# Kernel tuning notes

Measured on AMD Instinct MI355X. Metric: run time of the kernel, lower is better.

## Reference

```python
import jax, jax.numpy as jnp
import numpy as np

T_TYPES, N_ARGS, N_MAPS = 15, 73, 3
D, H, FF = 512, 8, 512
N_TOK = 3071
LN_EPS = 1e-5


def setup_inputs() -> dict:
    key = jax.random.key(0)
    ks = jax.random.split(key, 32)
    s = 0.02
    p = lambda i, shape: (jax.random.normal(ks[i], shape, dtype=jnp.float32) * s)
    inp = {
        'subtask_index_history': jax.random.randint(ks[0], (N_TOK,), 0, T_TYPES * N_ARGS * N_MAPS, dtype=jnp.int32),
        'seq_masks': jax.random.randint(ks[1], (N_TOK,), 0, 64, dtype=jnp.int32),
        'Wt': p(2, (D, T_TYPES)), 'bt': p(3, (D,)),
        'Wa': p(4, (D, N_ARGS)), 'ba': p(5, (D,)),
        'Wm': p(6, (D, N_MAPS)), 'bm': p(7, (D,)),
        'sos': jnp.zeros((D,), dtype=jnp.float32),
        'Wq': p(8, (D, D)), 'bq': p(9, (D,)),
        'Wk': p(10, (D, D)), 'bk': p(11, (D,)),
        'Wv': p(12, (D, D)), 'bv': p(13, (D,)),
        'Wo': p(14, (D, D)), 'bo': p(15, (D,)),
        'W1': p(16, (FF, D)), 'b1': p(17, (FF,)),
        'W2': p(18, (D, FF)), 'b2': p(19, (D,)),
        'g1': jnp.ones((D,), jnp.float32), 'be1': jnp.zeros((D,), jnp.float32),
        'g2': jnp.ones((D,), jnp.float32), 'be2': jnp.zeros((D,), jnp.float32),
    }
    return inp


def _layer_norm(x, g, b):
    mu = jnp.mean(x, axis=-1, keepdims=True)
    var = jnp.mean((x - mu) ** 2, axis=-1, keepdims=True)
    return (x - mu) * jax.lax.rsqrt(var + LN_EPS) * g + b


def _enc_layer(x, mask, Wq, bq, Wk, bk, Wv, bv, Wo, bo, W1, b1, W2, b2, g1, be1, g2, be2):
    # x: [L, D]; mask: [L, L] additive (0 / -inf). inputs_are_labels=True -> no attn residual.
    L = x.shape[0]
    dh = D // H
    q = (x @ Wq.T + bq).reshape(L, H, dh)
    k = (x @ Wk.T + bk).reshape(L, H, dh)
    v = (x @ Wv.T + bv).reshape(L, H, dh)
    scores = jnp.einsum('ihd,jhd->hij', q, k) / np.sqrt(dh) + mask[None]  # [H, L, L]
    pr = jax.nn.softmax(scores, axis=-1)
    o = jnp.einsum('hij,jhd->ihd', pr, v).reshape(L, D)
    a = o @ Wo.T + bo
    xa = _layer_norm(a, g1, be1)
    y = jax.nn.leaky_relu(xa @ W1.T + b1) @ W2.T + b2
    return _layer_norm(xa + y, g2, be2)


def reference(subtask_index_history, seq_masks, Wt, bt, Wa, ba, Wm, bm, sos,
              Wq, bq, Wk, bk, Wv, bv, Wo, bo, W1, b1, W2, b2, g1, be1, g2, be2):
    idx = subtask_index_history
    t = idx // (N_ARGS * N_MAPS)
    a = (idx // N_MAPS) % N_ARGS
    m = idx % N_MAPS
    # one-hot @ Linear == embedding gather + bias
    emb = (Wt.T[t] + bt) + (Wa.T[a] + ba) + (Wm.T[m] + bm)  # [N, D]
    x = jnp.concatenate([sos[None, :], emb], axis=0)  # [L, D]
    L = x.shape[0]
    batch_ids = jnp.cumsum((seq_masks == 0).astype(jnp.int32))
    bid = jnp.concatenate([jnp.array([-1], jnp.int32), batch_ids])  # SOS gets unique id
    ar = jnp.arange(L)
    allowed = (ar[None, :] == 0) | ((bid[:, None] == bid[None, :]) & (ar[None, :] < ar[:, None]))
    mask = jnp.where(allowed, 0.0, -jnp.inf).astype(jnp.float32)
    lp = (Wq, bq, Wk, bk, Wv, bv, Wo, bo, W1, b1, W2, b2, g1, be1, g2, be2)
    # original reuses transformer_layer_a for both calls
    x = _enc_layer(x, mask, *lp)
    x = _enc_layer(x, mask, *lp)
    return x
```

## Files before the change

kernel.cpp:

```cpp
#include <hip/hip_runtime.h>

typedef unsigned short ushort_t;
typedef unsigned int uint_t;

#define L_TOK 3072
#define DMODEL 512
#define WELEM 262144

using bf16x8 = __attribute__((ext_vector_type(8))) short;
using f32x4  = __attribute__((ext_vector_type(4))) float;

__device__ __forceinline__ float b2f(ushort_t u) {
    union { uint_t i; float f; } c; c.i = ((uint_t)u) << 16; return c.f;
}
__device__ __forceinline__ ushort_t f2b(float f) {
    union { float f; uint_t i; } c; c.f = f;
    uint_t x = c.i;
    return (ushort_t)((x + 0x7fffu + ((x >> 16) & 1u)) >> 16);
}

__global__ __launch_bounds__(256) void prologue_kernel(
    const float* __restrict__ Wq, const float* __restrict__ Wk, const float* __restrict__ Wv,
    const float* __restrict__ Wo, const float* __restrict__ W1, const float* __restrict__ W2,
    ushort_t* __restrict__ WB,
    const int* __restrict__ idx,
    const float* __restrict__ Wt, const float* __restrict__ bt,
    const float* __restrict__ Wa, const float* __restrict__ ba,
    const float* __restrict__ Wm, const float* __restrict__ bm,
    const float* __restrict__ sos, ushort_t* __restrict__ X,
    const int* __restrict__ seq, int* __restrict__ start)
{
    __shared__ int sbuf0[256];
    __shared__ int sbuf1[256];
    int bid = blockIdx.x;
    int tid = threadIdx.x;

    if (bid < 1536) {
        int gid = bid * 256 + tid;
        int mat = gid >> 16;
        int off = (gid & 65535) * 4;
        const float* src;
        switch (mat) {
            case 0: src = Wq; break;
            case 1: src = Wk; break;
            case 2: src = Wv; break;
            case 3: src = Wo; break;
            case 4: src = W1; break;
            default: src = W2; break;
        }
        float4 v = *reinterpret_cast<const float4*>(src + off);
        uint2 o;
        o.x = (uint_t)f2b(v.x) | ((uint_t)f2b(v.y) << 16);
        o.y = (uint_t)f2b(v.z) | ((uint_t)f2b(v.w) << 16);
        *reinterpret_cast<uint2*>(&WB[mat * WELEM + off]) = o;
    } else if (bid < 7680) {
        int gid = (bid - 1536) * 256 + tid;
        int tok = gid >> 9;
        int d = gid & 511;
        float val;
        if (tok == 0) {
            val = sos[d];
        } else {
            int id = idx[tok - 1];
            int t = id / 219;
            int a = (id / 3) % 73;
            int m = id % 3;
            val = Wt[d * 15 + t] + bt[d]
                + Wa[d * 73 + a] + ba[d]
                + Wm[d * 3 + m] + bm[d];
        }
        X[gid] = f2b(val);
    } else {
        int carry = 0;
        for (int c = 0; c < 12; c++) {
            int i = c * 256 + tid;
            int b;
            if (i <= 1) b = i;
            else b = (seq[i - 1] == 0) ? i : 0;
            sbuf0[tid] = b;
            __syncthreads();
            int* src = sbuf0;
            int* dst = sbuf1;
            for (int off = 1; off < 256; off <<= 1) {
                int v = src[tid];
                if (tid >= off) { int u = src[tid - off]; if (u > v) v = u; }
                dst[tid] = v;
                __syncthreads();
                int* t = src; src = dst; dst = t;
            }
            int val = src[tid] > carry ? src[tid] : carry;
            start[i] = val;
            int tot = src[255] > carry ? src[255] : carry;
            __syncthreads();
            carry = tot;
        }
    }
}

template<int RELU>
__global__ __launch_bounds__(256) void gemm512(
    const ushort_t* __restrict__ A,
    const ushort_t* __restrict__ Wp0, const ushort_t* __restrict__ Wp1, const ushort_t* __restrict__ Wp2,
    const float* __restrict__ bp0, const float* __restrict__ bp1, const float* __restrict__ bp2,
    ushort_t* __restrict__ Cp0, ushort_t* __restrict__ Cp1, ushort_t* __restrict__ Cp2)
{
    const ushort_t* W = Wp0; const float* bias = bp0; ushort_t* C = Cp0;
    if (blockIdx.z == 1) { W = Wp1; bias = bp1; C = Cp1; }
    else if (blockIdx.z == 2) { W = Wp2; bias = bp2; C = Cp2; }

    __shared__ ushort_t As[64 * 72];
    __shared__ ushort_t Bs[64 * 72];

    const int tid = threadIdx.x;
    const int lane = tid & 63;
    const int w = tid >> 6;
    const int lm = lane & 15;
    const int q4 = lane >> 4;

    const int m0 = blockIdx.x * 64;
    const int n0 = blockIdx.y * 64;

    f32x4 acc[4];
#pragma unroll
    for (int i = 0; i < 4; i++) acc[i] = (f32x4){0.f, 0.f, 0.f, 0.f};

    for (int k0 = 0; k0 < 512; k0 += 64) {
        for (int c = tid; c < 512; c += 256) {
            int row = c >> 3, col = (c & 7) << 3;
            uint4 va = *reinterpret_cast<const uint4*>(&A[(size_t)(m0 + row) * 512 + k0 + col]);
            *reinterpret_cast<uint4*>(&As[row * 72 + col]) = va;
            uint4 vb = *reinterpret_cast<const uint4*>(&W[(size_t)(n0 + row) * 512 + k0 + col]);
            *reinterpret_cast<uint4*>(&Bs[row * 72 + col]) = vb;
        }
        __syncthreads();
#pragma unroll
        for (int kk = 0; kk < 64; kk += 32) {
            bf16x8 af = *reinterpret_cast<const bf16x8*>(&As[(w * 16 + lm) * 72 + kk + q4 * 8]);
#pragma unroll
            for (int nt = 0; nt < 4; nt++) {
                bf16x8 bf = *reinterpret_cast<const bf16x8*>(&Bs[(nt * 16 + lm) * 72 + kk + q4 * 8]);
                acc[nt] = __builtin_amdgcn_mfma_f32_16x16x32_bf16(af, bf, acc[nt], 0, 0, 0);
            }
        }
        __syncthreads();
    }

#pragma unroll
    for (int nt = 0; nt < 4; nt++) {
        int col = n0 + nt * 16 + lm;
        float bv = bias[col];
#pragma unroll
        for (int r = 0; r < 4; r++) {
            int row = m0 + w * 16 + q4 * 4 + r;
            float v = acc[nt][r] + bv;
            if (RELU) v = (v > 0.f) ? v : 0.01f * v;
            C[(size_t)row * 512 + col] = f2b(v);
        }
    }
}

__global__ __launch_bounds__(256) void attn_mfma(
    const ushort_t* __restrict__ Q, const ushort_t* __restrict__ K,
    const ushort_t* __restrict__ V, const int* __restrict__ START,
    ushort_t* __restrict__ O)
{
    __shared__ ushort_t VtS[4][64 * 72];
    __shared__ ushort_t PsS[4][16 * 72];

    int w = threadIdx.x >> 6;
    int lane = threadIdx.x & 63;
    ushort_t* Vt = VtS[w];
    ushort_t* Ps = PsS[w];

    int gw = blockIdx.x * 4 + w;
    int tile = 191 - (gw >> 3);
    int h = gw & 7;
    int i0 = tile * 16;
    int lm = lane & 15;
    int q4 = lane >> 4;

    int iq0 = i0 + q4 * 4;
    int sq[4];
#pragma unroll
    for (int r = 0; r < 4; r++) sq[r] = START[iq0 + r];

    int lo = START[i0]; if (lo < 1) lo = 1;
    int nk = i0 + 16 - lo;

    const ushort_t* Qp = Q + (size_t)(i0 + lm) * 512 + h * 64 + q4 * 8;
    bf16x8 aQ0 = *reinterpret_cast<const bf16x8*>(Qp);
    bf16x8 aQ1 = *reinterpret_cast<const bf16x8*>(Qp + 32);

    float m_run[4], l_run[4];
    f32x4 oacc[4];
#pragma unroll
    for (int r = 0; r < 4; r++) { m_run[r] = -INFINITY; l_run[r] = 0.f; }
#pragma unroll
    for (int nt = 0; nt < 4; nt++) oacc[nt] = (f32x4){0.f, 0.f, 0.f, 0.f};

    for (int t0 = 0; t0 < nk; t0 += 64) {
        int tv = t0 + lane;
        int jv = (tv == 0) ? 0 : (lo + tv - 1);
        if (jv > L_TOK - 1) jv = L_TOK - 1;
        const uint4* vp = reinterpret_cast<const uint4*>(&V[(size_t)jv * 512 + h * 64]);
        uint4 vr[8];
#pragma unroll
        for (int c = 0; c < 8; c++) vr[c] = vp[c];

        int jn[4];
#pragma unroll
        for (int nt = 0; nt < 4; nt++) {
            int t = t0 + nt * 16 + lm;
            jn[nt] = (t == 0) ? 0 : (lo + t - 1);
        }
        f32x4 sacc[4];
#pragma unroll
        for (int nt = 0; nt < 4; nt++) sacc[nt] = (f32x4){0.f, 0.f, 0.f, 0.f};
#pragma unroll
        for (int nt = 0; nt < 4; nt++) {
            int jc = jn[nt] > L_TOK - 1 ? L_TOK - 1 : jn[nt];
            const ushort_t* Kp = K + (size_t)jc * 512 + h * 64 + q4 * 8;
            bf16x8 bK0 = *reinterpret_cast<const bf16x8*>(Kp);
            bf16x8 bK1 = *reinterpret_cast<const bf16x8*>(Kp + 32);
            sacc[nt] = __builtin_amdgcn_mfma_f32_16x16x32_bf16(aQ0, bK0, sacc[nt], 0, 0, 0);
            sacc[nt] = __builtin_amdgcn_mfma_f32_16x16x32_bf16(aQ1, bK1, sacc[nt], 0, 0, 0);
        }

#pragma unroll
        for (int c = 0; c < 8; c++) {
            uint_t ww[4] = {vr[c].x, vr[c].y, vr[c].z, vr[c].w};
#pragma unroll
            for (int e = 0; e < 4; e++) {
                int d0 = c * 8 + e * 2;
                Vt[d0 * 72 + lane] = (ushort_t)(ww[e] & 0xffffu);
                Vt[(d0 + 1) * 72 + lane] = (ushort_t)(ww[e] >> 16);
            }
        }

#pragma unroll
        for (int nt = 0; nt < 4; nt++) {
            int jju = jn[nt];
#pragma unroll
            for (int r = 0; r < 4; r++) {
                float s = sacc[nt][r] * 0.125f;
                bool val = (jju == 0) || (sq[r] <= jju && jju < iq0 + r);
                sacc[nt][r] = val ? s : -INFINITY;
            }
        }

        float mnew[4], alpha[4];
#pragma unroll
        for (int r = 0; r < 4; r++) {
            float mx = fmaxf(fmaxf(sacc[0][r], sacc[1][r]), fmaxf(sacc[2][r], sacc[3][r]));
            mx = fmaxf(mx, __shfl_xor(mx, 1));
            mx = fmaxf(mx, __shfl_xor(mx, 2));
            mx = fmaxf(mx, __shfl_xor(mx, 4));
            mx = fmaxf(mx, __shfl_xor(mx, 8));
            float mn = fmaxf(m_run[r], mx);
            mnew[r] = mn;
            alpha[r] = __expf(m_run[r] - mn);
        }

#pragma unroll
        for (int r = 0; r < 4; r++) {
            float rs = 0.f;
#pragma unroll
            for (int nt = 0; nt < 4; nt++) {
                float p = __expf(sacc[nt][r] - mnew[r]);
                rs += p;
                Ps[(q4 * 4 + r) * 72 + nt * 16 + lm] = f2b(p);
            }
            rs += __shfl_xor(rs, 1);
            rs += __shfl_xor(rs, 2);
            rs += __shfl_xor(rs, 4);
            rs += __shfl_xor(rs, 8);
            l_run[r] = l_run[r] * alpha[r] + rs;
            m_run[r] = mnew[r];
        }
#pragma unroll
        for (int nt = 0; nt < 4; nt++)
#pragma unroll
            for (int r = 0; r < 4; r++) oacc[nt][r] *= alpha[r];

        bf16x8 aP0 = *reinterpret_cast<const bf16x8*>(&Ps[lm * 72 + q4 * 8]);
        bf16x8 aP1 = *reinterpret_cast<const bf16x8*>(&Ps[lm * 72 + 32 + q4 * 8]);
#pragma unroll
        for (int nt = 0; nt < 4; nt++) {
            bf16x8 bV0 = *reinterpret_cast<const bf16x8*>(&Vt[(nt * 16 + lm) * 72 + q4 * 8]);
            bf16x8 bV1 = *reinterpret_cast<const bf16x8*>(&Vt[(nt * 16 + lm) * 72 + 32 + q4 * 8]);
            oacc[nt] = __builtin_amdgcn_mfma_f32_16x16x32_bf16(aP0, bV0, oacc[nt], 0, 0, 0);
            oacc[nt] = __builtin_amdgcn_mfma_f32_16x16x32_bf16(aP1, bV1, oacc[nt], 0, 0, 0);
        }
    }

#pragma unroll
    for (int r = 0; r < 4; r++) {
        float inv = (l_run[r] > 0.f) ? (1.f / l_run[r]) : 0.f;
#pragma unroll
        for (int nt = 0; nt < 4; nt++)
            O[(size_t)(iq0 + r) * 512 + h * 64 + nt * 16 + lm] = f2b(oacc[nt][r] * inv);
    }
}

template<int RESID, int F32OUT>
__global__ __launch_bounds__(256) void ln_kernel(
    const ushort_t* __restrict__ X, const ushort_t* __restrict__ R,
    const float* __restrict__ g, const float* __restrict__ be,
    void* __restrict__ outv)
{
    int tok = blockIdx.x * 4 + (threadIdx.x >> 6);
    int lane = threadIdx.x & 63;
    size_t base = (size_t)tok * 512 + lane * 8;

    float v[8];
    {
        uint4 ux = *reinterpret_cast<const uint4*>(&X[base]);
        uint_t ua[4] = {ux.x, ux.y, ux.z, ux.w};
#pragma unroll
        for (int p = 0; p < 4; p++) {
            v[2 * p] = b2f((ushort_t)(ua[p] & 0xffffu));
            v[2 * p + 1] = b2f((ushort_t)(ua[p] >> 16));
        }
        if (RESID) {
            uint4 ur = *reinterpret_cast<const uint4*>(&R[base]);
            uint_t ub[4] = {ur.x, ur.y, ur.z, ur.w};
#pragma unroll
            for (int p = 0; p < 4; p++) {
                v[2 * p] += b2f((ushort_t)(ub[p] & 0xffffu));
                v[2 * p + 1] += b2f((ushort_t)(ub[p] >> 16));
            }
        }
    }
    float sum = 0.f;
#pragma unroll
    for (int j = 0; j < 8; j++) sum += v[j];
#pragma unroll
    for (int off = 32; off > 0; off >>= 1) sum += __shfl_xor(sum, off);
    float mu = sum * (1.f / 512.f);
    float var = 0.f;
#pragma unroll
    for (int j = 0; j < 8; j++) { float d = v[j] - mu; var += d * d; }
#pragma unroll
    for (int off = 32; off > 0; off >>= 1) var += __shfl_xor(var, off);
    float rstd = rsqrtf(var * (1.f / 512.f) + 1e-5f);

    const float4* gp = reinterpret_cast<const float4*>(g);
    const float4* bp = reinterpret_cast<const float4*>(be);
    float4 g0 = gp[2 * lane], g1 = gp[2 * lane + 1];
    float4 b0 = bp[2 * lane], b1 = bp[2 * lane + 1];
    float gg[8] = {g0.x, g0.y, g0.z, g0.w, g1.x, g1.y, g1.z, g1.w};
    float bb[8] = {b0.x, b0.y, b0.z, b0.w, b1.x, b1.y, b1.z, b1.w};

    float o[8];
#pragma unroll
    for (int j = 0; j < 8; j++) o[j] = (v[j] - mu) * rstd * gg[j] + bb[j];

    if (F32OUT) {
        float* outf = (float*)outv;
        float4 o0 = {o[0], o[1], o[2], o[3]};
        float4 o1 = {o[4], o[5], o[6], o[7]};
        *reinterpret_cast<float4*>(&outf[base]) = o0;
        *reinterpret_cast<float4*>(&outf[base + 4]) = o1;
    } else {
        ushort_t* outb = (ushort_t*)outv;
        uint_t outp[4];
#pragma unroll
        for (int p = 0; p < 4; p++)
            outp[p] = (uint_t)f2b(o[2 * p]) | ((uint_t)f2b(o[2 * p + 1]) << 16);
        uint4 ov; ov.x = outp[0]; ov.y = outp[1]; ov.z = outp[2]; ov.w = outp[3];
        *reinterpret_cast<uint4*>(&outb[base]) = ov;
    }
}

extern "C" void kernel_launch(void* const* d_in, const int* in_sizes, int n_in,
                              void* d_out, int out_size, void* d_ws, size_t ws_size,
                              hipStream_t stream) {
    const int*   idx = (const int*)d_in[0];
    const int*   seq = (const int*)d_in[1];
    const float* Wt  = (const float*)d_in[2];
    const float* bt  = (const float*)d_in[3];
    const float* Wa  = (const float*)d_in[4];
    const float* ba  = (const float*)d_in[5];
    const float* Wm  = (const float*)d_in[6];
    const float* bm  = (const float*)d_in[7];
    const float* sos = (const float*)d_in[8];
    const float* Wq  = (const float*)d_in[9];
    const float* bq  = (const float*)d_in[10];
    const float* Wk  = (const float*)d_in[11];
    const float* bk  = (const float*)d_in[12];
    const float* Wv  = (const float*)d_in[13];
    const float* bv  = (const float*)d_in[14];
    const float* Wo  = (const float*)d_in[15];
    const float* bo  = (const float*)d_in[16];
    const float* W1  = (const float*)d_in[17];
    const float* b1  = (const float*)d_in[18];
    const float* W2  = (const float*)d_in[19];
    const float* b2  = (const float*)d_in[20];
    const float* g1  = (const float*)d_in[21];
    const float* be1 = (const float*)d_in[22];
    const float* g2  = (const float*)d_in[23];
    const float* be2 = (const float*)d_in[24];

    const size_t NB = (size_t)L_TOK * DMODEL;

    int* START = (int*)d_ws;
    ushort_t* WB = (ushort_t*)d_ws + 16384;
    ushort_t* WQc = WB + 0 * WELEM;
    ushort_t* WKc = WB + 1 * WELEM;
    ushort_t* WVc = WB + 2 * WELEM;
    ushort_t* WOc = WB + 3 * WELEM;
    ushort_t* W1c = WB + 4 * WELEM;
    ushort_t* W2c = WB + 5 * WELEM;
    ushort_t* bufs = WB + 6 * WELEM;
    ushort_t* B0 = bufs;
    ushort_t* B1 = bufs + 1 * NB;
    ushort_t* B2 = bufs + 2 * NB;
    ushort_t* B3 = bufs + 3 * NB;

    prologue_kernel<<<7681, 256, 0, stream>>>(
        Wq, Wk, Wv, Wo, W1, W2, WB,
        idx, Wt, bt, Wa, ba, Wm, bm, sos, B0,
        seq, START);

    for (int layer = 0; layer < 2; layer++) {
        gemm512<0><<<dim3(48, 8, 3), 256, 0, stream>>>(B0, WQc, WKc, WVc, bq, bk, bv, B1, B2, B3);
        attn_mfma<<<384, 256, 0, stream>>>(B1, B2, B3, START, B0);
        gemm512<0><<<dim3(48, 8, 1), 256, 0, stream>>>(B0, WOc, WOc, WOc, bo, bo, bo, B1, B1, B1);
        ln_kernel<0, 0><<<768, 256, 0, stream>>>(B1, B1, g1, be1, B2);
        gemm512<1><<<dim3(48, 8, 1), 256, 0, stream>>>(B2, W1c, W1c, W1c, b1, b1, b1, B1, B1, B1);
        gemm512<0><<<dim3(48, 8, 1), 256, 0, stream>>>(B1, W2c, W2c, W2c, b2, b2, b2, B3, B3, B3);
        if (layer == 0)
            ln_kernel<1, 0><<<768, 256, 0, stream>>>(B3, B2, g2, be2, B0);
        else
            ln_kernel<1, 1><<<768, 256, 0, stream>>>(B3, B2, g2, be2, d_out);
    }
}
```

Baseline: 275.5 us.

## Double-buffer LDS tiles in gemm512 with register prefetch of next K tile

The GEMM kernel now keeps two LDS buffers for A and W tiles. It prefetches the next K-slice from global memory into registers while MFMAs run on the current buffer, then writes it to the alternate buffer. This removes one barrier per K iteration and hides global load latency behind compute. In exchange it doubles shared memory per block and uses more registers, which may reduce occupancy.

```diff
diff --git a/kernel.cpp b/kernel.cpp
--- a/kernel.cpp
+++ b/kernel.cpp
@@ -108,8 +108,8 @@
     if (blockIdx.z == 1) { W = Wp1; bias = bp1; C = Cp1; }
     else if (blockIdx.z == 2) { W = Wp2; bias = bp2; C = Cp2; }
 
-    __shared__ ushort_t As[64 * 72];
-    __shared__ ushort_t Bs[64 * 72];
+    __shared__ ushort_t As[2 * 64 * 72];
+    __shared__ ushort_t Bs[2 * 64 * 72];
 
     const int tid = threadIdx.x;
     const int lane = tid & 63;
@@ -120,29 +120,60 @@
     const int m0 = blockIdx.x * 64;
     const int n0 = blockIdx.y * 64;
 
+    const int row0 = tid >> 3;
+    const int colc = (tid & 7) << 3;
+    const ushort_t* Arow0 = A + (size_t)(m0 + row0) * 512 + colc;
+    const ushort_t* Arow1 = Arow0 + (size_t)32 * 512;
+    const ushort_t* Brow0 = W + (size_t)(n0 + row0) * 512 + colc;
+    const ushort_t* Brow1 = Brow0 + (size_t)32 * 512;
+    const int lds0 = row0 * 72 + colc;
+    const int lds1 = (row0 + 32) * 72 + colc;
+
     f32x4 acc[4];
 #pragma unroll
     for (int i = 0; i < 4; i++) acc[i] = (f32x4){0.f, 0.f, 0.f, 0.f};
 
-    for (int k0 = 0; k0 < 512; k0 += 64) {
-        for (int c = tid; c < 512; c += 256) {
-            int row = c >> 3, col = (c & 7) << 3;
-            uint4 va = *reinterpret_cast<const uint4*>(&A[(size_t)(m0 + row) * 512 + k0 + col]);
-            *reinterpret_cast<uint4*>(&As[row * 72 + col]) = va;
-            uint4 vb = *reinterpret_cast<const uint4*>(&W[(size_t)(n0 + row) * 512 + k0 + col]);
-            *reinterpret_cast<uint4*>(&Bs[row * 72 + col]) = vb;
-        }
-        __syncthreads();
+    uint4 a0 = *reinterpret_cast<const uint4*>(Arow0);
+    uint4 a1 = *reinterpret_cast<const uint4*>(Arow1);
+    uint4 b0 = *reinterpret_cast<const uint4*>(Brow0);
+    uint4 b1 = *reinterpret_cast<const uint4*>(Brow1);
+    *reinterpret_cast<uint4*>(&As[lds0]) = a0;
+    *reinterpret_cast<uint4*>(&As[lds1]) = a1;
+    *reinterpret_cast<uint4*>(&Bs[lds0]) = b0;
+    *reinterpret_cast<uint4*>(&Bs[lds1]) = b1;
+    __syncthreads();
+
+#pragma unroll
+    for (int it = 0; it < 8; it++) {
+        const int cur = (it & 1) * 4608;
+        const int alt = ((it & 1) ^ 1) * 4608;
+        const int nxt = (it + 1) * 64;
+
+        uint4 na0, na1, nb0, nb1;
+        if (it < 7) {
+            na0 = *reinterpret_cast<const uint4*>(Arow0 + nxt);
+            na1 = *reinterpret_cast<const uint4*>(Arow1 + nxt);
+            nb0 = *reinterpret_cast<const uint4*>(Brow0 + nxt);
+            nb1 = *reinterpret_cast<const uint4*>(Brow1 + nxt);
+        }
+
 #pragma unroll
         for (int kk = 0; kk < 64; kk += 32) {
-            bf16x8 af = *reinterpret_cast<const bf16x8*>(&As[(w * 16 + lm) * 72 + kk + q4 * 8]);
+            bf16x8 af = *reinterpret_cast<const bf16x8*>(&As[cur + (w * 16 + lm) * 72 + kk + q4 * 8]);
 #pragma unroll
             for (int nt = 0; nt < 4; nt++) {
-                bf16x8 bf = *reinterpret_cast<const bf16x8*>(&Bs[(nt * 16 + lm) * 72 + kk + q4 * 8]);
+                bf16x8 bf = *reinterpret_cast<const bf16x8*>(&Bs[cur + (nt * 16 + lm) * 72 + kk + q4 * 8]);
                 acc[nt] = __builtin_amdgcn_mfma_f32_16x16x32_bf16(af, bf, acc[nt], 0, 0, 0);
             }
         }
-        __syncthreads();
+
+        if (it < 7) {
+            *reinterpret_cast<uint4*>(&As[alt + lds0]) = na0;
+            *reinterpret_cast<uint4*>(&As[alt + lds1]) = na1;
+            *reinterpret_cast<uint4*>(&Bs[alt + lds0]) = nb0;
+            *reinterpret_cast<uint4*>(&Bs[alt + lds1]) = nb1;
+            __syncthreads();
+        }
     }
 
 #pragma unroll
```

Result: faster. 253.9 us (-7.8%).

## Double-buffer GEMM LDS tiles with register prefetch and shrink M tile to 32

Applied to the files above, without the earlier changes.

The 512-K GEMM now prefetches the next K-slice from global memory into registers while MFMAs run on the current LDS buffer, then writes it into an alternate LDS buffer. This leaves one barrier per iteration instead of two. The block tile shrinks from 64x64 to 32x64, with each wave computing a 16x32 sub-tile, so twice as many blocks launch for better occupancy on the small 3072-row problem. In exchange, LDS use rises and each block does fewer MFMAs per B-tile load, which lowers reuse.

```diff
diff --git a/kernel.cpp b/kernel.cpp
--- a/kernel.cpp
+++ b/kernel.cpp
@@ -108,50 +108,81 @@
     if (blockIdx.z == 1) { W = Wp1; bias = bp1; C = Cp1; }
     else if (blockIdx.z == 2) { W = Wp2; bias = bp2; C = Cp2; }
 
-    __shared__ ushort_t As[64 * 72];
-    __shared__ ushort_t Bs[64 * 72];
+    __shared__ ushort_t As[2 * 32 * 72];
+    __shared__ ushort_t Bs[2 * 64 * 72];
 
     const int tid = threadIdx.x;
     const int lane = tid & 63;
     const int w = tid >> 6;
     const int lm = lane & 15;
     const int q4 = lane >> 4;
-
-    const int m0 = blockIdx.x * 64;
+    const int r0 = (w & 1) * 16;
+    const int c0 = (w >> 1) * 32;
+
+    const int m0 = blockIdx.x * 32;
     const int n0 = blockIdx.y * 64;
 
-    f32x4 acc[4];
-#pragma unroll
-    for (int i = 0; i < 4; i++) acc[i] = (f32x4){0.f, 0.f, 0.f, 0.f};
-
-    for (int k0 = 0; k0 < 512; k0 += 64) {
-        for (int c = tid; c < 512; c += 256) {
-            int row = c >> 3, col = (c & 7) << 3;
-            uint4 va = *reinterpret_cast<const uint4*>(&A[(size_t)(m0 + row) * 512 + k0 + col]);
-            *reinterpret_cast<uint4*>(&As[row * 72 + col]) = va;
-            uint4 vb = *reinterpret_cast<const uint4*>(&W[(size_t)(n0 + row) * 512 + k0 + col]);
-            *reinterpret_cast<uint4*>(&Bs[row * 72 + col]) = vb;
-        }
-        __syncthreads();
+    const int srow = tid >> 3;
+    const int scol = (tid & 7) << 3;
+    const ushort_t* Arow = A + (size_t)(m0 + srow) * 512 + scol;
+    const ushort_t* Brow0 = W + (size_t)(n0 + srow) * 512 + scol;
+    const ushort_t* Brow1 = Brow0 + (size_t)32 * 512;
+    const int ldsA = srow * 72 + scol;
+    const int ldsB0 = srow * 72 + scol;
+    const int ldsB1 = (srow + 32) * 72 + scol;
+
+    f32x4 acc[2];
+    acc[0] = (f32x4){0.f, 0.f, 0.f, 0.f};
+    acc[1] = (f32x4){0.f, 0.f, 0.f, 0.f};
+
+    uint4 a0 = *reinterpret_cast<const uint4*>(Arow);
+    uint4 b0 = *reinterpret_cast<const uint4*>(Brow0);
+    uint4 b1 = *reinterpret_cast<const uint4*>(Brow1);
+    *reinterpret_cast<uint4*>(&As[ldsA]) = a0;
+    *reinterpret_cast<uint4*>(&Bs[ldsB0]) = b0;
+    *reinterpret_cast<uint4*>(&Bs[ldsB1]) = b1;
+    __syncthreads();
+
+#pragma unroll
+    for (int it = 0; it < 8; it++) {
+        const int curA = (it & 1) * 2304;
+        const int altA = ((it & 1) ^ 1) * 2304;
+        const int curB = (it & 1) * 4608;
+        const int altB = ((it & 1) ^ 1) * 4608;
+        const int nxt = (it + 1) * 64;
+
+        uint4 na, nb0, nb1;
+        if (it < 7) {
+            na = *reinterpret_cast<const uint4*>(Arow + nxt);
+            nb0 = *reinterpret_cast<const uint4*>(Brow0 + nxt);
+            nb1 = *reinterpret_cast<const uint4*>(Brow1 + nxt);
+        }
+
 #pragma unroll
         for (int kk = 0; kk < 64; kk += 32) {
-            bf16x8 af = *reinterpret_cast<const bf16x8*>(&As[(w * 16 + lm) * 72 + kk + q4 * 8]);
-#pragma unroll
-            for (int nt = 0; nt < 4; nt++) {
-                bf16x8 bf = *reinterpret_cast<const bf16x8*>(&Bs[(nt * 16 + lm) * 72 + kk + q4 * 8]);
+            bf16x8 af = *reinterpret_cast<const bf16x8*>(&As[curA + (r0 + lm) * 72 + kk + q4 * 8]);
+#pragma unroll
+            for (int nt = 0; nt < 2; nt++) {
+                bf16x8 bf = *reinterpret_cast<const bf16x8*>(&Bs[curB + (c0 + nt * 16 + lm) * 72 + kk + q4 * 8]);
                 acc[nt] = __builtin_amdgcn_mfma_f32_16x16x32_bf16(af, bf, acc[nt], 0, 0, 0);
             }
         }
-        __syncthreads();
-    }
-
-#pragma unroll
-    for (int nt = 0; nt < 4; nt++) {
-        int col = n0 + nt * 16 + lm;
+
+        if (it < 7) {
+            *reinterpret_cast<uint4*>(&As[altA + ldsA]) = na;
+            *reinterpret_cast<uint4*>(&Bs[altB + ldsB0]) = nb0;
+            *reinterpret_cast<uint4*>(&Bs[altB + ldsB1]) = nb1;
+            __syncthreads();
+        }
+    }
+
+#pragma unroll
+    for (int nt = 0; nt < 2; nt++) {
+        int col = n0 + c0 + nt * 16 + lm;
         float bv = bias[col];
 #pragma unroll
         for (int r = 0; r < 4; r++) {
-            int row = m0 + w * 16 + q4 * 4 + r;
+            int row = m0 + r0 + q4 * 4 + r;
             float v = acc[nt][r] + bv;
             if (RELU) v = (v > 0.f) ? v : 0.01f * v;
             C[(size_t)row * 512 + col] = f2b(v);
@@ -423,12 +454,12 @@
         seq, START);
 
     for (int layer = 0; layer < 2; layer++) {
-        gemm512<0><<<dim3(48, 8, 3), 256, 0, stream>>>(B0, WQc, WKc, WVc, bq, bk, bv, B1, B2, B3);
+        gemm512<0><<<dim3(96, 8, 3), 256, 0, stream>>>(B0, WQc, WKc, WVc, bq, bk, bv, B1, B2, B3);
         attn_mfma<<<384, 256, 0, stream>>>(B1, B2, B3, START, B0);
-        gemm512<0><<<dim3(48, 8, 1), 256, 0, stream>>>(B0, WOc, WOc, WOc, bo, bo, bo, B1, B1, B1);
+        gemm512<0><<<dim3(96, 8, 1), 256, 0, stream>>>(B0, WOc, WOc, WOc, bo, bo, bo, B1, B1, B1);
         ln_kernel<0, 0><<<768, 256, 0, stream>>>(B1, B1, g1, be1, B2);
-        gemm512<1><<<dim3(48, 8, 1), 256, 0, stream>>>(B2, W1c, W1c, W1c, b1, b1, b1, B1, B1, B1);
-        gemm512<0><<<dim3(48, 8, 1), 256, 0, stream>>>(B1, W2c, W2c, W2c, b2, b2, b2, B3, B3, B3);
+        gemm512<1><<<dim3(96, 8, 1), 256, 0, stream>>>(B2, W1c, W1c, W1c, b1, b1, b1, B1, B1, B1);
+        gemm512<0><<<dim3(96, 8, 1), 256, 0, stream>>>(B1, W2c, W2c, W2c, b2, b2, b2, B3, B3, B3);
         if (layer == 0)
             ln_kernel<1, 0><<<768, 256, 0, stream>>>(B3, B2, g2, be2, B0);
         else
```

After: 253.6 us, median of 2. 1.09x faster.

## Drop LDS staging in gemm512, load MFMA fragments directly from global

Applied to the files above, without the earlier changes.

The GEMM kernel no longer stages A and W tiles in shared memory with barriers. Each wave now loads its bf16 fragments straight from global memory into registers and accumulates a 16x32 sub-tile. The block tile shrinks from 64x64 to 32x64, which doubles the grid to raise parallelism across CUs. This removes LDS traffic and syncthreads, at the cost of less data reuse inside a block, so more global/L2 reads per MFMA.

```diff
diff --git a/kernel.cpp b/kernel.cpp
--- a/kernel.cpp
+++ b/kernel.cpp
@@ -108,51 +108,54 @@
     if (blockIdx.z == 1) { W = Wp1; bias = bp1; C = Cp1; }
     else if (blockIdx.z == 2) { W = Wp2; bias = bp2; C = Cp2; }
 
-    __shared__ ushort_t As[64 * 72];
-    __shared__ ushort_t Bs[64 * 72];
-
-    const int tid = threadIdx.x;
-    const int lane = tid & 63;
-    const int w = tid >> 6;
+    const int lane = threadIdx.x & 63;
+    const int w = threadIdx.x >> 6;
     const int lm = lane & 15;
     const int q4 = lane >> 4;
-
-    const int m0 = blockIdx.x * 64;
+    const int r0 = (w & 1) * 16;
+    const int c0 = (w >> 1) * 32;
+
+    const int m0 = blockIdx.x * 32;
     const int n0 = blockIdx.y * 64;
 
-    f32x4 acc[4];
-#pragma unroll
-    for (int i = 0; i < 4; i++) acc[i] = (f32x4){0.f, 0.f, 0.f, 0.f};
-
-    for (int k0 = 0; k0 < 512; k0 += 64) {
-        for (int c = tid; c < 512; c += 256) {
-            int row = c >> 3, col = (c & 7) << 3;
-            uint4 va = *reinterpret_cast<const uint4*>(&A[(size_t)(m0 + row) * 512 + k0 + col]);
-            *reinterpret_cast<uint4*>(&As[row * 72 + col]) = va;
-            uint4 vb = *reinterpret_cast<const uint4*>(&W[(size_t)(n0 + row) * 512 + k0 + col]);
-            *reinterpret_cast<uint4*>(&Bs[row * 72 + col]) = vb;
-        }
-        __syncthreads();
-#pragma unroll
-        for (int kk = 0; kk < 64; kk += 32) {
-            bf16x8 af = *reinterpret_cast<const bf16x8*>(&As[(w * 16 + lm) * 72 + kk + q4 * 8]);
-#pragma unroll
-            for (int nt = 0; nt < 4; nt++) {
-                bf16x8 bf = *reinterpret_cast<const bf16x8*>(&Bs[(nt * 16 + lm) * 72 + kk + q4 * 8]);
-                acc[nt] = __builtin_amdgcn_mfma_f32_16x16x32_bf16(af, bf, acc[nt], 0, 0, 0);
-            }
-        }
-        __syncthreads();
-    }
-
-#pragma unroll
-    for (int nt = 0; nt < 4; nt++) {
-        int col = n0 + nt * 16 + lm;
+    const ushort_t* Ap  = A + (size_t)(m0 + r0 + lm) * 512 + q4 * 8;
+    const ushort_t* Bp0 = W + (size_t)(n0 + c0 + lm) * 512 + q4 * 8;
+    const ushort_t* Bp1 = Bp0 + (size_t)16 * 512;
+
+    f32x4 acc0 = (f32x4){0.f, 0.f, 0.f, 0.f};
+    f32x4 acc1 = (f32x4){0.f, 0.f, 0.f, 0.f};
+
+#pragma unroll 2
+    for (int it = 0; it < 8; it++) {
+        const int ko = it * 64;
+        bf16x8 a0  = *reinterpret_cast<const bf16x8*>(Ap + ko);
+        bf16x8 a1  = *reinterpret_cast<const bf16x8*>(Ap + ko + 32);
+        bf16x8 b00 = *reinterpret_cast<const bf16x8*>(Bp0 + ko);
+        bf16x8 b10 = *reinterpret_cast<const bf16x8*>(Bp1 + ko);
+        bf16x8 b01 = *reinterpret_cast<const bf16x8*>(Bp0 + ko + 32);
+        bf16x8 b11 = *reinterpret_cast<const bf16x8*>(Bp1 + ko + 32);
+        acc0 = __builtin_amdgcn_mfma_f32_16x16x32_bf16(a0, b00, acc0, 0, 0, 0);
+        acc1 = __builtin_amdgcn_mfma_f32_16x16x32_bf16(a0, b10, acc1, 0, 0, 0);
+        acc0 = __builtin_amdgcn_mfma_f32_16x16x32_bf16(a1, b01, acc0, 0, 0, 0);
+        acc1 = __builtin_amdgcn_mfma_f32_16x16x32_bf16(a1, b11, acc1, 0, 0, 0);
+    }
+
+    {
+        int col = n0 + c0 + lm;
         float bv = bias[col];
 #pragma unroll
         for (int r = 0; r < 4; r++) {
-            int row = m0 + w * 16 + q4 * 4 + r;
-            float v = acc[nt][r] + bv;
+            int row = m0 + r0 + q4 * 4 + r;
+            float v = acc0[r] + bv;
+            if (RELU) v = (v > 0.f) ? v : 0.01f * v;
+            C[(size_t)row * 512 + col] = f2b(v);
+        }
+        col = n0 + c0 + 16 + lm;
+        bv = bias[col];
+#pragma unroll
+        for (int r = 0; r < 4; r++) {
+            int row = m0 + r0 + q4 * 4 + r;
+            float v = acc1[r] + bv;
             if (RELU) v = (v > 0.f) ? v : 0.01f * v;
             C[(size_t)row * 512 + col] = f2b(v);
         }
@@ -423,12 +426,12 @@
         seq, START);
 
     for (int layer = 0; layer < 2; layer++) {
-        gemm512<0><<<dim3(48, 8, 3), 256, 0, stream>>>(B0, WQc, WKc, WVc, bq, bk, bv, B1, B2, B3);
+        gemm512<0><<<dim3(96, 8, 3), 256, 0, stream>>>(B0, WQc, WKc, WVc, bq, bk, bv, B1, B2, B3);
         attn_mfma<<<384, 256, 0, stream>>>(B1, B2, B3, START, B0);
-        gemm512<0><<<dim3(48, 8, 1), 256, 0, stream>>>(B0, WOc, WOc, WOc, bo, bo, bo, B1, B1, B1);
+        gemm512<0><<<dim3(96, 8, 1), 256, 0, stream>>>(B0, WOc, WOc, WOc, bo, bo, bo, B1, B1, B1);
         ln_kernel<0, 0><<<768, 256, 0, stream>>>(B1, B1, g1, be1, B2);
-        gemm512<1><<<dim3(48, 8, 1), 256, 0, stream>>>(B2, W1c, W1c, W1c, b1, b1, b1, B1, B1, B1);
-        gemm512<0><<<dim3(48, 8, 1), 256, 0, stream>>>(B1, W2c, W2c, W2c, b2, b2, b2, B3, B3, B3);
+        gemm512<1><<<dim3(96, 8, 1), 256, 0, stream>>>(B2, W1c, W1c, W1c, b1, b1, b1, B1, B1, B1);
+        gemm512<0><<<dim3(96, 8, 1), 256, 0, stream>>>(B1, W2c, W2c, W2c, b2, b2, b2, B3, B3, B3);
         if (layer == 0)
             ln_kernel<1, 0><<<768, 256, 0, stream>>>(B3, B2, g2, be2, B0);
         else
```

Measured after the change: 402.5 us. +46.1%, slower.
